# Kernel tuning notes

Measured on AMD Instinct MI355X. Metric: run time of the kernel, lower is better.

Reference implementation:

```python
import jax, jax.numpy as jnp
import numpy as np

T, N, E, IN, H, H2, H3, B, AF = 12, 50000, 800000, 12, 128, 64, 32, 4096, 10
BN_EPS = 1e-5


def _gin_mlp(h, w1, b1, g, be, rm, rv, w2, b2):
    # Linear -> ReLU -> BatchNorm1d (eval: running stats) -> Dropout(eval=id) -> Linear -> ReLU
    h = jax.nn.relu(h @ w1.T + b1)
    h = (h - rm) * (g * jax.lax.rsqrt(rv + BN_EPS)) + be
    return jax.nn.relu(h @ w2.T + b2)


def _gin_conv(x, edge_src, edge_dst, mlp_params):
    # GINConv with eps=0: MLP(x + sum_{j in N(i)} x_j), scatter-add over edges
    agg = jax.ops.segment_sum(x[edge_src], edge_dst, num_segments=x.shape[0])
    return _gin_mlp(x + agg, *mlp_params)


def _gru(xs, wih, whh, bih, bhh):
    # torch.nn.GRU, 1 layer, h0 = zeros. xs: [T, N, H_in]
    h0 = jnp.zeros((xs.shape[1], whh.shape[1]), xs.dtype)

    def step(h, x):
        gi = x @ wih.T + bih
        gh = h @ whh.T + bhh
        ir, iz, inn = jnp.split(gi, 3, axis=-1)
        hr, hz, hn = jnp.split(gh, 3, axis=-1)
        r = jax.nn.sigmoid(ir + hr)
        z = jax.nn.sigmoid(iz + hz)
        n = jnp.tanh(inn + r * hn)
        h_new = (1.0 - z) * n + z * h
        return h_new, h_new

    h_last, ys = jax.lax.scan(step, h0, xs)
    return ys, h_last


def _forward(floats, edge_src, edge_dst, target_idx):
    (x_seq, apart_feature,
     c1_w1, c1_b1, c1_g, c1_be, c1_rm, c1_rv, c1_w2, c1_b2,
     c2_w1, c2_b1, c2_g, c2_be, c2_rm, c2_rv, c2_w2, c2_b2,
     gru_wih, gru_whh, gru_bih, gru_bhh,
     fc1_w, fc1_b, fc2_w, fc2_b, fc3_w, fc3_b) = floats

    c1 = (c1_w1, c1_b1, c1_g, c1_be, c1_rm, c1_rv, c1_w2, c1_b2)
    c2 = (c2_w1, c2_b1, c2_g, c2_be, c2_rm, c2_rv, c2_w2, c2_b2)

    # conv1 per time slot (lax.map keeps the E x H gather intermediate per-step)
    # extra torch.relu after conv1 is a no-op since the MLP ends in ReLU
    emb = jax.lax.map(lambda xt: _gin_conv(xt, edge_src, edge_dst, c1), x_seq)
    seq, _ = _gru(emb, gru_wih, gru_whh, gru_bih, gru_bhh)
    emb2 = jax.lax.map(lambda xt: _gin_conv(xt, edge_src, edge_dst, c2), seq)
    _, h_last = _gru(emb2, gru_wih, gru_whh, gru_bih, gru_bhh)  # same GRU weights reused

    feat = jnp.concatenate([h_last[target_idx], apart_feature], axis=1)
    h = jax.nn.leaky_relu(feat @ fc1_w.T + fc1_b, negative_slope=0.1)
    h = jax.nn.leaky_relu(h @ fc2_w.T + fc2_b, negative_slope=0.05)
    return h @ fc3_w.T + fc3_b  # [B, 1]


def setup_inputs() -> dict:
    key = jax.random.key(0)
    ks = jax.random.split(key, 24)
    f32 = jnp.float32
    w = lambda i, shape, fan: jax.random.normal(ks[i], shape, f32) * (1.0 / np.sqrt(fan))
    return {
        "x_seq": jax.random.normal(ks[0], (T, N, IN), f32),
        "apart_feature": jax.random.normal(ks[1], (B, AF), f32),
        "edge_src": jax.random.randint(ks[2], (E,), 0, N, jnp.int32),
        "edge_dst": jax.random.randint(ks[3], (E,), 0, N, jnp.int32),
        "target_idx": jax.random.randint(ks[4], (B,), 0, N, jnp.int32),
        # conv1 MLP
        "c1_w1": w(5, (H, IN), IN), "c1_b1": jnp.zeros((H,), f32),
        "c1_g": jnp.ones((H,), f32), "c1_be": jnp.zeros((H,), f32),
        "c1_rm": jnp.zeros((H,), f32), "c1_rv": jnp.ones((H,), f32),
        "c1_w2": w(6, (H, H), H), "c1_b2": jnp.zeros((H,), f32),
        # conv2 MLP
        "c2_w1": w(7, (H, H), H), "c2_b1": jnp.zeros((H,), f32),
        "c2_g": jnp.ones((H,), f32), "c2_be": jnp.zeros((H,), f32),
        "c2_rm": jnp.zeros((H,), f32), "c2_rv": jnp.ones((H,), f32),
        "c2_w2": w(8, (H, H), H), "c2_b2": jnp.zeros((H,), f32),
        # shared GRU
        "gru_wih": w(9, (3 * H, H), H), "gru_whh": w(10, (3 * H, H), H),
        "gru_bih": jnp.zeros((3 * H,), f32), "gru_bhh": jnp.zeros((3 * H,), f32),
        # head
        "fc1_w": w(11, (H2, H + AF), H + AF), "fc1_b": jnp.zeros((H2,), f32),
        "fc2_w": w(12, (H3, H2), H2), "fc2_b": jnp.zeros((H3,), f32),
        "fc3_w": w(13, (1, H3), H3), "fc3_b": jnp.zeros((1,), f32),
    }


def reference(x_seq, apart_feature,
              c1_w1, c1_b1, c1_g, c1_be, c1_rm, c1_rv, c1_w2, c1_b2,
              c2_w1, c2_b1, c2_g, c2_be, c2_rm, c2_rv, c2_w2, c2_b2,
              gru_wih, gru_whh, gru_bih, gru_bhh,
              fc1_w, fc1_b, fc2_w, fc2_b, fc3_w, fc3_b,
              edge_src, edge_dst, target_idx):
    floats = (x_seq, apart_feature,
              c1_w1, c1_b1, c1_g, c1_be, c1_rm, c1_rv, c1_w2, c1_b2,
              c2_w1, c2_b1, c2_g, c2_be, c2_rm, c2_rv, c2_w2, c2_b2,
              gru_wih, gru_whh, gru_bih, gru_bhh,
              fc1_w, fc1_b, fc2_w, fc2_b, fc3_w, fc3_b)
    return _forward(floats, edge_src, edge_dst, target_idx)
```

## Files before the change

kernel.cpp:

```cpp
#include <hip/hip_runtime.h>

#define T_STEPS 12
#define NN      50000
#define EE      800000
#define IN_F    12
#define HID     128
#define G3      384
#define BB      4096
#define AF_     10
#define BN_EPS  1e-5f
#define LPAD    136
#define NBLK    ((NN + 63) / 64)

typedef unsigned short ushort_t;
typedef __attribute__((ext_vector_type(8))) short bf16x8;
typedef __attribute__((ext_vector_type(4))) float f32x4;

#define MFMA(a, b, c) __builtin_amdgcn_mfma_f32_16x16x32_bf16((a), (b), (c), 0, 0, 0)
#define L2E 1.4426950408889634f

__device__ inline float b2f(ushort_t u) { return __uint_as_float(((unsigned)u) << 16); }
__device__ inline float b2f_lo(unsigned u) { return __uint_as_float(u << 16); }
__device__ inline float b2f_hi(unsigned u) { return __uint_as_float(u & 0xffff0000u); }
__device__ inline ushort_t f2b(float f) {
    unsigned u = __float_as_uint(f);
    return (ushort_t)((u + 0x7fffu + ((u >> 16) & 1u)) >> 16);
}
__device__ inline float sigm(float x) {
    return __builtin_amdgcn_rcpf(1.f + __builtin_amdgcn_exp2f(-x * L2E));
}
__device__ inline float ftanh(float x) {
    float xx = fminf(fmaxf(x, -15.f), 15.f);
    float t = __builtin_amdgcn_exp2f(2.f * L2E * xx);
    return (t - 1.f) * __builtin_amdgcn_rcpf(t + 1.f);
}
__device__ inline void v4add(float4& a, const float4 b) {
    a.x += b.x; a.y += b.y; a.z += b.z; a.w += b.w;
}

#define ALIGN_UP(x) (((x) + 255) & ~(size_t)255)
#define SZ_DEG    ALIGN_UP((size_t)NN * 4)
#define SZ_RP     ALIGN_UP((size_t)(NN + 1) * 4)
#define SZ_CUR    ALIGN_UP((size_t)NN * 4)
#define SZ_COL    ALIGN_UP((size_t)EE * 4)
#define SZ_X12A   ALIGN_UP((size_t)T_STEPS * NN * IN_F * 4)
#define SZ_EMB    ALIGN_UP((size_t)T_STEPS * NN * HID * 2)
#define SZ_NHB    ALIGN_UP((size_t)NN * HID * 2)
#define SZ_W128   ALIGN_UP((size_t)HID * HID * 2)
#define SZ_WGRU   ALIGN_UP((size_t)G3 * HID * 2)
#define WS_NEED   (SZ_DEG + SZ_RP + SZ_CUR + SZ_COL + SZ_X12A + SZ_EMB + 3 * SZ_NHB + 3 * SZ_W128 + 2 * SZ_WGRU)

__device__ __align__(256) char g_static_pool[WS_NEED];

__global__ void zero_out_kernel(float* out, int n) {
    int i = blockIdx.x * blockDim.x + threadIdx.x;
    if (i < n) out[i] = 0.f;
}

__global__ void cvt5_kernel(const float* s0, ushort_t* d0, int n0,
                            const float* s1, ushort_t* d1, int n1,
                            const float* s2, ushort_t* d2, int n2,
                            const float* s3, ushort_t* d3, int n3,
                            const float* s4, ushort_t* d4, int n4) {
    int i = blockIdx.x * blockDim.x + threadIdx.x;
    if (i < n0) d0[i] = f2b(s0[i]);
    i -= n0;
    if (i >= 0 && i < n1) d1[i] = f2b(s1[i]);
    i -= n1;
    if (i >= 0 && i < n2) d2[i] = f2b(s2[i]);
    i -= n2;
    if (i >= 0 && i < n3) d3[i] = f2b(s3[i]);
    i -= n3;
    if (i >= 0 && i < n4) d4[i] = f2b(s4[i]);
}

__global__ void init_kernel(int* deg, ushort_t* h1, ushort_t* h2) {
    int i = blockIdx.x * blockDim.x + threadIdx.x;
    if (i < NN) deg[i] = 0;
    if (i < NN * HID) { h1[i] = 0; h2[i] = 0; }
}

__global__ void hist_kernel(const int* __restrict__ dst, int* __restrict__ deg, int E) {
    int e = blockIdx.x * blockDim.x + threadIdx.x;
    if (e < E) {
        unsigned d = (unsigned)dst[e];
        if (d < NN) atomicAdd(&deg[d], 1);
    }
}

__global__ __launch_bounds__(1024) void scan_kernel(const int* __restrict__ deg,
                                                    int* __restrict__ row_ptr,
                                                    int* __restrict__ cursor, int n) {
    __shared__ int wsum[16];
    __shared__ int carry_s;
    int tid = threadIdx.x;
    int wid = tid >> 6, lane = tid & 63;
    if (tid == 0) { carry_s = 0; row_ptr[0] = 0; }
    __syncthreads();
    for (int base = 0; base < n; base += 1024) {
        int i = base + tid;
        int v = (i < n) ? deg[i] : 0;
        int x = v;
#pragma unroll
        for (int off = 1; off < 64; off <<= 1) {
            int t = __shfl_up(x, (unsigned)off);
            if (lane >= off) x += t;
        }
        if (lane == 63) wsum[wid] = x;
        __syncthreads();
        if (tid == 0) {
            int a = 0;
#pragma unroll
            for (int w = 0; w < 16; ++w) { int t = wsum[w]; wsum[w] = a; a += t; }
        }
        __syncthreads();
        int incl = carry_s + wsum[wid] + x;
        if (i < n) {
            row_ptr[i + 1] = incl;
            cursor[i] = incl - v;
        }
        __syncthreads();
        if (tid == 1023) carry_s = incl;
        __syncthreads();
    }
}

__global__ void scatter_kernel(const int* __restrict__ src, const int* __restrict__ dst,
                               int* __restrict__ cursor, int* __restrict__ col, int E) {
    int e = blockIdx.x * blockDim.x + threadIdx.x;
    if (e < E) {
        unsigned d = (unsigned)dst[e];
        if (d < NN) {
            int pos = atomicAdd(&cursor[d], 1);
            if ((unsigned)pos < (unsigned)EE) col[pos] = src[e];
        }
    }
}

__global__ void agg12v_kernel(const float* __restrict__ x_seq, const int* __restrict__ rp,
                              const int* __restrict__ col, float* __restrict__ xin12_all, int E) {
    int g = blockIdx.x * blockDim.x + threadIdx.x;
    if (g >= T_STEPS * NN) return;
    int t = g / NN;
    int i = g - t * NN;
    const float* xt = x_seq + (size_t)t * NN * IN_F;
    const float4* pr = (const float4*)(xt + (size_t)i * IN_F);
    float4 a0 = pr[0], a1 = pr[1], a2 = pr[2];
    int e0 = rp[i], e1 = rp[i + 1];
    if (e1 > E) e1 = E;
    int e = e0;
    for (; e + 1 < e1; e += 2) {
        unsigned c0 = (unsigned)col[e], c1 = (unsigned)col[e + 1];
        c0 = (c0 < NN) ? c0 : 0; c1 = (c1 < NN) ? c1 : 0;
        const float4* p0 = (const float4*)(xt + (size_t)c0 * IN_F);
        const float4* p1 = (const float4*)(xt + (size_t)c1 * IN_F);
        float4 b0 = p0[0], b1 = p0[1], b2 = p0[2];
        float4 d0 = p1[0], d1 = p1[1], d2 = p1[2];
        v4add(a0, b0); v4add(a1, b1); v4add(a2, b2);
        v4add(a0, d0); v4add(a1, d1); v4add(a2, d2);
    }
    for (; e < e1; ++e) {
        unsigned c = (unsigned)col[e];
        if (c < NN) {
            const float4* pn = (const float4*)(xt + (size_t)c * IN_F);
            v4add(a0, pn[0]); v4add(a1, pn[1]); v4add(a2, pn[2]);
        }
    }
    float4* po = (float4*)(xin12_all + (size_t)g * IN_F);
    po[0] = a0; po[1] = a1; po[2] = a2;
}

__global__ __launch_bounds__(512) void conv1c_all_kernel(const float* __restrict__ xin12_all,
                                                         ushort_t* __restrict__ emb,
                                                         const float* __restrict__ W1, const float* __restrict__ b1,
                                                         const float* __restrict__ gg, const float* __restrict__ be,
                                                         const float* __restrict__ rm, const float* __restrict__ rv,
                                                         const ushort_t* __restrict__ w2b, const float* __restrict__ b2) {
    __shared__ float xs[64][IN_F + 1];
    __shared__ ushort_t l1[64][LPAD];
    int t = blockIdx.y;
    const float* xt = xin12_all + (size_t)t * NN * IN_F;
    ushort_t* et = emb + (size_t)t * NN * HID;
    int tid = threadIdx.x;
    int r0 = blockIdx.x * 64;
    for (int u = tid; u < 64 * IN_F; u += 512) {
        int r = u / IN_F, f = u - r * IN_F;
        int row = r0 + r;
        xs[r][f] = (row < NN) ? xt[(size_t)row * IN_F + f] : 0.f;
    }
    __syncthreads();
    {
        int j = tid & 127, rb = tid >> 7;
        float sc = gg[j] * rsqrtf(rv[j] + BN_EPS);
        float sh = be[j] - rm[j] * sc;
        float bj = b1[j];
        float wreg[IN_F];
#pragma unroll
        for (int k = 0; k < IN_F; ++k) wreg[k] = W1[j * IN_F + k];
#pragma unroll
        for (int q = 0; q < 16; ++q) {
            int r = rb + q * 4;
            float s = bj;
#pragma unroll
            for (int k = 0; k < IN_F; ++k) s += xs[r][k] * wreg[k];
            s = fmaxf(s, 0.f);
            l1[r][j] = f2b(s * sc + sh);
        }
    }
    __syncthreads();
    {
        int wave = tid >> 6, lane = tid & 63, li = lane & 15, ks = lane >> 4;
        int jc = wave * 16 + li;
        const ushort_t* pw = w2b + (size_t)jc * HID + ks * 8;
        f32x4 A0 = {0,0,0,0}, A1 = {0,0,0,0}, A2 = {0,0,0,0}, A3 = {0,0,0,0};
#pragma unroll
        for (int k0 = 0; k0 < HID; k0 += 32) {
            bf16x8 wf = *(const bf16x8*)(pw + k0);
            bf16x8 a0 = *(const bf16x8*)&l1[li][ks * 8 + k0];
            bf16x8 a1 = *(const bf16x8*)&l1[li + 16][ks * 8 + k0];
            bf16x8 a2 = *(const bf16x8*)&l1[li + 32][ks * 8 + k0];
            bf16x8 a3 = *(const bf16x8*)&l1[li + 48][ks * 8 + k0];
            A0 = MFMA(a0, wf, A0); A1 = MFMA(a1, wf, A1);
            A2 = MFMA(a2, wf, A2); A3 = MFMA(a3, wf, A3);
        }
        float bj = b2[jc];
#pragma unroll
        for (int q = 0; q < 4; ++q) {
            int rA = r0 + ks * 4 + q, rB = rA + 16, rC = rA + 32, rD = rA + 48;
            if (rA < NN) et[(size_t)rA * HID + jc] = f2b(fmaxf(A0[q] + bj, 0.f));
            if (rB < NN) et[(size_t)rB * HID + jc] = f2b(fmaxf(A1[q] + bj, 0.f));
            if (rC < NN) et[(size_t)rC * HID + jc] = f2b(fmaxf(A2[q] + bj, 0.f));
            if (rD < NN) et[(size_t)rD * HID + jc] = f2b(fmaxf(A3[q] + bj, 0.f));
        }
    }
}

__device__ __forceinline__ void gru_body(const ushort_t* __restrict__ x,
                                         ushort_t* __restrict__ h,
                                         const ushort_t* __restrict__ wih,
                                         const ushort_t* __restrict__ whh,
                                         const float* __restrict__ bih,
                                         const float* __restrict__ bhh, int blk) {
    int tid = threadIdx.x;
    int wave = tid >> 6, lane = tid & 63, li = lane & 15, ks = lane >> 4;
    int r0 = blk * 64;
    int jc = wave * 16 + li;
    const ushort_t* px[4];
    const ushort_t* ph[4];
#pragma unroll
    for (int tt = 0; tt < 4; ++tt) {
        int ra = min(r0 + tt * 16 + li, NN - 1);
        px[tt] = x + (size_t)ra * HID + ks * 8;
        ph[tt] = h + (size_t)ra * HID + ks * 8;
    }
    const ushort_t* pwr = wih + (size_t)jc * HID + ks * 8;
    const ushort_t* pwz = wih + (size_t)(HID + jc) * HID + ks * 8;
    const ushort_t* pwn = wih + (size_t)(2 * HID + jc) * HID + ks * 8;
    const ushort_t* pvr = whh + (size_t)jc * HID + ks * 8;
    const ushort_t* pvz = whh + (size_t)(HID + jc) * HID + ks * 8;
    const ushort_t* pvn = whh + (size_t)(2 * HID + jc) * HID + ks * 8;
    f32x4 Ir[4], Iz[4], In[4], Hr[4], Hz[4], Hn[4];
#pragma unroll
    for (int tt = 0; tt < 4; ++tt) {
        Ir[tt] = (f32x4){0,0,0,0}; Iz[tt] = (f32x4){0,0,0,0}; In[tt] = (f32x4){0,0,0,0};
        Hr[tt] = (f32x4){0,0,0,0}; Hz[tt] = (f32x4){0,0,0,0}; Hn[tt] = (f32x4){0,0,0,0};
    }
#pragma unroll
    for (int k0 = 0; k0 < HID; k0 += 32) {
        bf16x8 wr = *(const bf16x8*)(pwr + k0);
        bf16x8 wz = *(const bf16x8*)(pwz + k0);
        bf16x8 wn = *(const bf16x8*)(pwn + k0);
        bf16x8 vr = *(const bf16x8*)(pvr + k0);
        bf16x8 vz = *(const bf16x8*)(pvz + k0);
        bf16x8 vn = *(const bf16x8*)(pvn + k0);
#pragma unroll
        for (int tt = 0; tt < 4; ++tt) {
            bf16x8 xf = *(const bf16x8*)(px[tt] + k0);
            bf16x8 hf = *(const bf16x8*)(ph[tt] + k0);
            Ir[tt] = MFMA(xf, wr, Ir[tt]);
            Iz[tt] = MFMA(xf, wz, Iz[tt]);
            In[tt] = MFMA(xf, wn, In[tt]);
            Hr[tt] = MFMA(hf, vr, Hr[tt]);
            Hz[tt] = MFMA(hf, vz, Hz[tt]);
            Hn[tt] = MFMA(hf, vn, Hn[tt]);
        }
    }
    float bi_r = bih[jc], bi_z = bih[HID + jc], bi_n = bih[2 * HID + jc];
    float bh_r = bhh[jc], bh_z = bhh[HID + jc], bh_n = bhh[2 * HID + jc];
    float hold[4][4];
#pragma unroll
    for (int tt = 0; tt < 4; ++tt)
#pragma unroll
        for (int q = 0; q < 4; ++q) {
            int rr = min(r0 + tt * 16 + ks * 4 + q, NN - 1);
            hold[tt][q] = b2f(h[(size_t)rr * HID + jc]);
        }
    __syncthreads();
#pragma unroll
    for (int tt = 0; tt < 4; ++tt)
#pragma unroll
        for (int q = 0; q < 4; ++q) {
            int row = r0 + tt * 16 + ks * 4 + q;
            float rg = sigm(Ir[tt][q] + bi_r + Hr[tt][q] + bh_r);
            float zg = sigm(Iz[tt][q] + bi_z + Hz[tt][q] + bh_z);
            float ng = ftanh(In[tt][q] + bi_n + rg * (Hn[tt][q] + bh_n));
            float hv = (1.f - zg) * ng + zg * hold[tt][q];
            if (row < NN) h[(size_t)row * HID + jc] = f2b(hv);
        }
}

__device__ __forceinline__ void mega2_body(const ushort_t* __restrict__ xin2,
                                           ushort_t* __restrict__ h2,
                                           const ushort_t* __restrict__ w1b, const float* __restrict__ b1,
                                           const float* __restrict__ gg, const float* __restrict__ be,
                                           const float* __restrict__ rm, const float* __restrict__ rv,
                                           const ushort_t* __restrict__ w2b, const float* __restrict__ b2,
                                           const ushort_t* __restrict__ wih, const ushort_t* __restrict__ whh,
                                           const float* __restrict__ bih, const float* __restrict__ bhh, int blk) {
    __shared__ ushort_t bufA[64][LPAD];
    __shared__ ushort_t bufB[64][LPAD];
    int tid = threadIdx.x;
    int wave = tid >> 6, lane = tid & 63, li = lane & 15, ks = lane >> 4;
    int r0 = blk * 64;
    int jc = wave * 16 + li;
    f32x4 Hr[4], Hz[4], Hn[4], C1[4];
#pragma unroll
    for (int tt = 0; tt < 4; ++tt) {
        Hr[tt] = (f32x4){0,0,0,0}; Hz[tt] = (f32x4){0,0,0,0};
        Hn[tt] = (f32x4){0,0,0,0}; C1[tt] = (f32x4){0,0,0,0};
    }
    {
        const ushort_t* pw1 = w1b + (size_t)jc * HID + ks * 8;
        const ushort_t* pvr = whh + (size_t)jc * HID + ks * 8;
        const ushort_t* pvz = whh + (size_t)(HID + jc) * HID + ks * 8;
        const ushort_t* pvn = whh + (size_t)(2 * HID + jc) * HID + ks * 8;
        const ushort_t* pa[4];
        const ushort_t* ph[4];
#pragma unroll
        for (int tt = 0; tt < 4; ++tt) {
            int ra = min(r0 + tt * 16 + li, NN - 1);
            pa[tt] = xin2 + (size_t)ra * HID + ks * 8;
            ph[tt] = h2 + (size_t)ra * HID + ks * 8;
        }
#pragma unroll
        for (int k0 = 0; k0 < HID; k0 += 32) {
            bf16x8 w1f = *(const bf16x8*)(pw1 + k0);
            bf16x8 vr = *(const bf16x8*)(pvr + k0);
            bf16x8 vz = *(const bf16x8*)(pvz + k0);
            bf16x8 vn = *(const bf16x8*)(pvn + k0);
#pragma unroll
            for (int tt = 0; tt < 4; ++tt) {
                bf16x8 af = *(const bf16x8*)(pa[tt] + k0);
                bf16x8 hf = *(const bf16x8*)(ph[tt] + k0);
                C1[tt] = MFMA(af, w1f, C1[tt]);
                Hr[tt] = MFMA(hf, vr, Hr[tt]);
                Hz[tt] = MFMA(hf, vz, Hz[tt]);
                Hn[tt] = MFMA(hf, vn, Hn[tt]);
            }
        }
    }
    float hold[4][4];
#pragma unroll
    for (int tt = 0; tt < 4; ++tt)
#pragma unroll
        for (int q = 0; q < 4; ++q) {
            int rr = min(r0 + tt * 16 + ks * 4 + q, NN - 1);
            hold[tt][q] = b2f(h2[(size_t)rr * HID + jc]);
        }
    {
        float sc = gg[jc] * rsqrtf(rv[jc] + BN_EPS);
        float sh = be[jc] - rm[jc] * sc;
        float bj = b1[jc];
#pragma unroll
        for (int tt = 0; tt < 4; ++tt)
#pragma unroll
            for (int q = 0; q < 4; ++q)
                bufB[tt * 16 + ks * 4 + q][jc] = f2b(fmaxf(C1[tt][q] + bj, 0.f) * sc + sh);
    }
    __syncthreads();
    {
        const ushort_t* pw2 = w2b + (size_t)jc * HID + ks * 8;
        f32x4 C2[4];
#pragma unroll
        for (int tt = 0; tt < 4; ++tt) C2[tt] = (f32x4){0,0,0,0};
#pragma unroll
        for (int k0 = 0; k0 < HID; k0 += 32) {
            bf16x8 wf = *(const bf16x8*)(pw2 + k0);
#pragma unroll
            for (int tt = 0; tt < 4; ++tt) {
                bf16x8 af = *(const bf16x8*)&bufB[li + 16 * tt][ks * 8 + k0];
                C2[tt] = MFMA(af, wf, C2[tt]);
            }
        }
        float bj = b2[jc];
#pragma unroll
        for (int tt = 0; tt < 4; ++tt)
#pragma unroll
            for (int q = 0; q < 4; ++q)
                bufA[tt * 16 + ks * 4 + q][jc] = f2b(fmaxf(C2[tt][q] + bj, 0.f));
    }
    __syncthreads();
    {
        const ushort_t* pwr = wih + (size_t)jc * HID + ks * 8;
        const ushort_t* pwz = wih + (size_t)(HID + jc) * HID + ks * 8;
        const ushort_t* pwn = wih + (size_t)(2 * HID + jc) * HID + ks * 8;
        f32x4 Ir[4], Iz[4], In[4];
#pragma unroll
        for (int tt = 0; tt < 4; ++tt) {
            Ir[tt] = (f32x4){0,0,0,0}; Iz[tt] = (f32x4){0,0,0,0}; In[tt] = (f32x4){0,0,0,0};
        }
#pragma unroll
        for (int k0 = 0; k0 < HID; k0 += 32) {
            bf16x8 wr = *(const bf16x8*)(pwr + k0);
            bf16x8 wz = *(const bf16x8*)(pwz + k0);
            bf16x8 wn = *(const bf16x8*)(pwn + k0);
#pragma unroll
            for (int tt = 0; tt < 4; ++tt) {
                bf16x8 xf = *(const bf16x8*)&bufA[li + 16 * tt][ks * 8 + k0];
                Ir[tt] = MFMA(xf, wr, Ir[tt]);
                Iz[tt] = MFMA(xf, wz, Iz[tt]);
                In[tt] = MFMA(xf, wn, In[tt]);
            }
        }
        float bi_r = bih[jc], bi_z = bih[HID + jc], bi_n = bih[2 * HID + jc];
        float bh_r = bhh[jc], bh_z = bhh[HID + jc], bh_n = bhh[2 * HID + jc];
#pragma unroll
        for (int tt = 0; tt < 4; ++tt)
#pragma unroll
            for (int q = 0; q < 4; ++q) {
                int row = r0 + tt * 16 + ks * 4 + q;
                float rg = sigm(Ir[tt][q] + bi_r + Hr[tt][q] + bh_r);
                float zg = sigm(Iz[tt][q] + bi_z + Hz[tt][q] + bh_z);
                float ng = ftanh(In[tt][q] + bi_n + rg * (Hn[tt][q] + bh_n));
                float hv = (1.f - zg) * ng + zg * hold[tt][q];
                if (row < NN) h2[(size_t)row * HID + jc] = f2b(hv);
            }
    }
}

__global__ __launch_bounds__(512) void gru_step_kernel(const ushort_t* __restrict__ x, ushort_t* __restrict__ h,
                                                       const ushort_t* __restrict__ wih, const ushort_t* __restrict__ whh,
                                                       const float* __restrict__ bih, const float* __restrict__ bhh) {
    gru_body(x, h, wih, whh, bih, bhh, blockIdx.x);
}

__global__ __launch_bounds__(512) void mega2_kernel(const ushort_t* __restrict__ xin2, ushort_t* __restrict__ h2,
                                                    const ushort_t* __restrict__ w1b, const float* __restrict__ b1,
                                                    const float* __restrict__ gg, const float* __restrict__ be,
                                                    const float* __restrict__ rm, const float* __restrict__ rv,
                                                    const ushort_t* __restrict__ w2b, const float* __restrict__ b2,
                                                    const ushort_t* __restrict__ wih, const ushort_t* __restrict__ whh,
                                                    const float* __restrict__ bih, const float* __restrict__ bhh) {
    mega2_body(xin2, h2, w1b, b1, gg, be, rm, rv, w2b, b2, wih, whh, bih, bhh, blockIdx.x);
}

__global__ __launch_bounds__(512) void fused_mg_kernel(const ushort_t* __restrict__ xin2, ushort_t* __restrict__ h2,
                                                       const ushort_t* __restrict__ w1b, const float* __restrict__ b1,
                                                       const float* __restrict__ gg, const float* __restrict__ be,
                                                       const float* __restrict__ rm, const float* __restrict__ rv,
                                                       const ushort_t* __restrict__ w2b, const float* __restrict__ b2,
                                                       const ushort_t* __restrict__ wih, const ushort_t* __restrict__ whh,
                                                       const float* __restrict__ bih, const float* __restrict__ bhh,
                                                       const ushort_t* __restrict__ emb_next, ushort_t* __restrict__ h1) {
    int b = blockIdx.x;
    if (b < NBLK) {
        mega2_body(xin2, h2, w1b, b1, gg, be, rm, rv, w2b, b2, wih, whh, bih, bhh, b);
    } else {
        gru_body(emb_next, h1, wih, whh, bih, bhh, b - NBLK);
    }
}

__global__ __launch_bounds__(256) void agg128b_kernel(const ushort_t* __restrict__ x,
                                                      const int* __restrict__ rp,
                                                      const int* __restrict__ col,
                                                      ushort_t* __restrict__ out, int E) {
    int node = (blockIdx.x * 256 + threadIdx.x) >> 6;
    int lane = threadIdx.x & 63;
    if (node >= NN) return;
    unsigned v = *(const unsigned*)(x + (size_t)node * HID + lane * 2);
    float s0 = b2f_lo(v);
    float s1 = b2f_hi(v);
    int e0 = rp[node], e1 = rp[node + 1];
    if (e1 > E) e1 = E;
    int e = e0;
    for (; e + 3 < e1; e += 4) {
        unsigned c0 = (unsigned)col[e], c1 = (unsigned)col[e + 1];
        unsigned c2 = (unsigned)col[e + 2], c3 = (unsigned)col[e + 3];
        c0 = (c0 < NN) ? c0 : 0; c1 = (c1 < NN) ? c1 : 0;
        c2 = (c2 < NN) ? c2 : 0; c3 = (c3 < NN) ? c3 : 0;
        unsigned u0 = *(const unsigned*)(x + (size_t)c0 * HID + lane * 2);
        unsigned u1 = *(const unsigned*)(x + (size_t)c1 * HID + lane * 2);
        unsigned u2 = *(const unsigned*)(x + (size_t)c2 * HID + lane * 2);
        unsigned u3 = *(const unsigned*)(x + (size_t)c3 * HID + lane * 2);
        s0 += b2f_lo(u0) + b2f_lo(u1) + b2f_lo(u2) + b2f_lo(u3);
        s1 += b2f_hi(u0) + b2f_hi(u1) + b2f_hi(u2) + b2f_hi(u3);
    }
    for (; e < e1; ++e) {
        unsigned c = (unsigned)col[e];
        if (c < NN) {
            unsigned u = *(const unsigned*)(x + (size_t)c * HID + lane * 2);
            s0 += b2f_lo(u);
            s1 += b2f_hi(u);
        }
    }
    unsigned o = (unsigned)f2b(s0) | ((unsigned)f2b(s1) << 16);
    *(unsigned*)(out + (size_t)node * HID + lane * 2) = o;
}

__global__ __launch_bounds__(64) void head_kernel(const ushort_t* __restrict__ h2, const int* __restrict__ tidx,
                                                  const float* __restrict__ apart,
                                                  const float* __restrict__ w1, const float* __restrict__ b1,
                                                  const float* __restrict__ w2, const float* __restrict__ b2,
                                                  const float* __restrict__ w3, const float* __restrict__ b3,
                                                  float* __restrict__ out) {
    __shared__ float feat[HID + AF_];
    __shared__ float o1[64];
    __shared__ float o2[32];
    int b = blockIdx.x;
    int t = threadIdx.x;
    unsigned node = (unsigned)tidx[b];
    if (node >= NN) node = 0;
    for (int k = t; k < HID; k += 64) feat[k] = b2f(h2[(size_t)node * HID + k]);
    if (t < AF_) feat[HID + t] = apart[(size_t)b * AF_ + t];
    __syncthreads();
    {
        float s = b1[t];
        for (int k = 0; k < HID + AF_; ++k) s += feat[k] * w1[t * (HID + AF_) + k];
        o1[t] = (s > 0.f) ? s : 0.1f * s;
    }
    __syncthreads();
    if (t < 32) {
        float s = b2[t];
        for (int k = 0; k < 64; ++k) s += o1[k] * w2[t * 64 + k];
        o2[t] = (s > 0.f) ? s : 0.05f * s;
    }
    __syncthreads();
    if (t == 0) {
        float s = b3[0];
        for (int k = 0; k < 32; ++k) s += o2[k] * w3[k];
        out[b] = s;
    }
}

extern "C" void kernel_launch(void* const* d_in, const int* in_sizes, int n_in,
                              void* d_out, int out_size, void* d_ws, size_t ws_size,
                              hipStream_t stream) {
    int ie_src = -1, ie_dst = -1, ie_tidx = -1, iw0 = -1;
    bool ok = false;
    if (n_in >= 31 && in_sizes[0] == T_STEPS * NN * IN_F && in_sizes[1] == BB * AF_) {
        if (in_sizes[2] > 100000 && in_sizes[3] == in_sizes[2] && in_sizes[4] == BB &&
            in_sizes[5] == HID * IN_F && in_sizes[11] == HID * HID &&
            in_sizes[21] == G3 * HID && in_sizes[22] == G3 * HID &&
            in_sizes[25] == 64 * (HID + AF_)) {
            ie_src = 2; ie_dst = 3; ie_tidx = 4; iw0 = 5; ok = true;
        } else if (in_sizes[2] == HID * IN_F && in_sizes[8] == HID * HID &&
                   in_sizes[18] == G3 * HID && in_sizes[19] == G3 * HID &&
                   in_sizes[22] == 64 * (HID + AF_) &&
                   in_sizes[28] > 100000 && in_sizes[29] == in_sizes[28] && in_sizes[30] == BB) {
            iw0 = 2; ie_src = 28; ie_dst = 29; ie_tidx = 30; ok = true;
        }
    }
    if (!ok) {
        zero_out_kernel<<<(out_size + 255) / 256, 256, 0, stream>>>((float*)d_out, out_size);
        return;
    }

    const float* x_seq  = (const float*)d_in[0];
    const float* apart  = (const float*)d_in[1];
    const int*   e_src  = (const int*)d_in[ie_src];
    const int*   e_dst  = (const int*)d_in[ie_dst];
    const int*   t_idx  = (const int*)d_in[ie_tidx];
    const float* c1_w1 = (const float*)d_in[iw0 + 0];
    const float* c1_b1 = (const float*)d_in[iw0 + 1];
    const float* c1_g  = (const float*)d_in[iw0 + 2];
    const float* c1_be = (const float*)d_in[iw0 + 3];
    const float* c1_rm = (const float*)d_in[iw0 + 4];
    const float* c1_rv = (const float*)d_in[iw0 + 5];
    const float* c1_w2 = (const float*)d_in[iw0 + 6];
    const float* c1_b2 = (const float*)d_in[iw0 + 7];
    const float* c2_w1 = (const float*)d_in[iw0 + 8];
    const float* c2_b1 = (const float*)d_in[iw0 + 9];
    const float* c2_g  = (const float*)d_in[iw0 + 10];
    const float* c2_be = (const float*)d_in[iw0 + 11];
    const float* c2_rm = (const float*)d_in[iw0 + 12];
    const float* c2_rv = (const float*)d_in[iw0 + 13];
    const float* c2_w2 = (const float*)d_in[iw0 + 14];
    const float* c2_b2 = (const float*)d_in[iw0 + 15];
    const float* g_wih = (const float*)d_in[iw0 + 16];
    const float* g_whh = (const float*)d_in[iw0 + 17];
    const float* g_bih = (const float*)d_in[iw0 + 18];
    const float* g_bhh = (const float*)d_in[iw0 + 19];
    const float* f1_w  = (const float*)d_in[iw0 + 20];
    const float* f1_b  = (const float*)d_in[iw0 + 21];
    const float* f2_w  = (const float*)d_in[iw0 + 22];
    const float* f2_b  = (const float*)d_in[iw0 + 23];
    const float* f3_w  = (const float*)d_in[iw0 + 24];
    const float* f3_b  = (const float*)d_in[iw0 + 25];

    int E = in_sizes[ie_src];
    if (E > EE) E = EE;

    char* base;
    if (ws_size >= WS_NEED) {
        base = (char*)d_ws;
    } else {
        void* sp = nullptr;
        hipGetSymbolAddress(&sp, HIP_SYMBOL(g_static_pool));
        if (sp == nullptr) {
            zero_out_kernel<<<(out_size + 255) / 256, 256, 0, stream>>>((float*)d_out, out_size);
            return;
        }
        base = (char*)sp;
    }
    size_t off = 0;
    auto nxt = [&](size_t bytes) { char* p = base + off; off += bytes; return p; };
    int*      deg      = (int*)nxt(SZ_DEG);
    int*      row_ptr  = (int*)nxt(SZ_RP);
    int*      cursor   = (int*)nxt(SZ_CUR);
    int*      col      = (int*)nxt(SZ_COL);
    float*    xin12a   = (float*)nxt(SZ_X12A);
    ushort_t* emb      = (ushort_t*)nxt(SZ_EMB);
    ushort_t* xin2     = (ushort_t*)nxt(SZ_NHB);
    ushort_t* h1       = (ushort_t*)nxt(SZ_NHB);
    ushort_t* h2       = (ushort_t*)nxt(SZ_NHB);
    ushort_t* wb_c1w2  = (ushort_t*)nxt(SZ_W128);
    ushort_t* wb_c2w1  = (ushort_t*)nxt(SZ_W128);
    ushort_t* wb_c2w2  = (ushort_t*)nxt(SZ_W128);
    ushort_t* wb_wih   = (ushort_t*)nxt(SZ_WGRU);
    ushort_t* wb_whh   = (ushort_t*)nxt(SZ_WGRU);

    const int NW = 3 * HID * HID + 2 * G3 * HID;
    cvt5_kernel<<<(NW + 255) / 256, 256, 0, stream>>>(c1_w2, wb_c1w2, HID * HID,
                                                      c2_w1, wb_c2w1, HID * HID,
                                                      c2_w2, wb_c2w2, HID * HID,
                                                      g_wih, wb_wih, G3 * HID,
                                                      g_whh, wb_whh, G3 * HID);

    init_kernel<<<(NN * HID + 255) / 256, 256, 0, stream>>>(deg, h1, h2);

    hist_kernel<<<(E + 255) / 256, 256, 0, stream>>>(e_dst, deg, E);
    scan_kernel<<<1, 1024, 0, stream>>>(deg, row_ptr, cursor, NN);
    scatter_kernel<<<(E + 255) / 256, 256, 0, stream>>>(e_src, e_dst, cursor, col, E);

    agg12v_kernel<<<(T_STEPS * NN + 255) / 256, 256, 0, stream>>>(x_seq, row_ptr, col, xin12a, E);
    conv1c_all_kernel<<<dim3(NBLK, T_STEPS), 512, 0, stream>>>(xin12a, emb,
                                                               c1_w1, c1_b1, c1_g, c1_be, c1_rm, c1_rv,
                                                               wb_c1w2, c1_b2);

    gru_step_kernel<<<NBLK, 512, 0, stream>>>(emb, h1, wb_wih, wb_whh, g_bih, g_bhh);
    agg128b_kernel<<<(NN * 64 + 255) / 256, 256, 0, stream>>>(h1, row_ptr, col, xin2, E);
    for (int t = 0; t < T_STEPS - 1; ++t) {
        fused_mg_kernel<<<2 * NBLK, 512, 0, stream>>>(xin2, h2,
                                                      wb_c2w1, c2_b1, c2_g, c2_be, c2_rm, c2_rv,
                                                      wb_c2w2, c2_b2,
                                                      wb_wih, wb_whh, g_bih, g_bhh,
                                                      emb + (size_t)(t + 1) * NN * HID, h1);
        agg128b_kernel<<<(NN * 64 + 255) / 256, 256, 0, stream>>>(h1, row_ptr, col, xin2, E);
    }
    mega2_kernel<<<NBLK, 512, 0, stream>>>(xin2, h2,
                                           wb_c2w1, c2_b1, c2_g, c2_be, c2_rm, c2_rv,
                                           wb_c2w2, c2_b2,
                                           wb_wih, wb_whh, g_bih, g_bhh);

    head_kernel<<<BB, 64, 0, stream>>>(h2, t_idx, apart, f1_w, f1_b, f2_w, f2_b, f3_w, f3_b, (float*)d_out);
}
```

Before: 2.351 ms.

## Interleave per-step conv1 and input aggregation into layer-2 recurrence kernels

The upfront all-timestep input aggregation and conv1 launches are split per time plane. Each plane's work is folded into the fusedA kernel alongside the 128-wide neighbour aggregation of the recurrent loop, so that lightweight conv1 work fills the GPU during the latency-bound aggregation steps. Shared memory moves to explicit pools so different bodies can share one kernel. The cost is more complex block dispatch and a larger shared footprint in the aggregation kernel, which may lower its occupancy.

```diff
diff --git a/kernel.cpp b/kernel.cpp
--- a/kernel.cpp
+++ b/kernel.cpp
@@ -11,6 +11,8 @@
 #define BN_EPS  1e-5f
 #define LPAD    136
 #define NBLK    ((NN + 63) / 64)
+#define AGGB    ((NN + 7) / 8)
+#define AGVB    ((NN + 511) / 512)
 
 typedef unsigned short ushort_t;
 typedef __attribute__((ext_vector_type(8))) short bf16x8;
@@ -49,6 +51,9 @@
 #define SZ_W128   ALIGN_UP((size_t)HID * HID * 2)
 #define SZ_WGRU   ALIGN_UP((size_t)G3 * HID * 2)
 #define WS_NEED   (SZ_DEG + SZ_RP + SZ_CUR + SZ_COL + SZ_X12A + SZ_EMB + 3 * SZ_NHB + 3 * SZ_W128 + 2 * SZ_WGRU)
+
+#define POOL_C1   (64 * (IN_F + 1) * 4 + 64 * LPAD * 2)
+#define POOL_M2   (2 * 64 * LPAD * 2)
 
 __device__ __align__(256) char g_static_pool[WS_NEED];
 
@@ -137,13 +142,13 @@
     }
 }
 
-__global__ void agg12v_kernel(const float* __restrict__ x_seq, const int* __restrict__ rp,
-                              const int* __restrict__ col, float* __restrict__ xin12_all, int E) {
-    int g = blockIdx.x * blockDim.x + threadIdx.x;
-    if (g >= T_STEPS * NN) return;
-    int t = g / NN;
-    int i = g - t * NN;
-    const float* xt = x_seq + (size_t)t * NN * IN_F;
+__device__ __forceinline__ void agg12v_body(const float* __restrict__ x_seq, const int* __restrict__ rp,
+                                            const int* __restrict__ col, float* __restrict__ xin12_all,
+                                            int E, int plane, int blk) {
+    int tid = threadIdx.x;
+    int i = blk * 512 + tid;
+    if (i >= NN) return;
+    const float* xt = x_seq + (size_t)plane * NN * IN_F;
     const float4* pr = (const float4*)(xt + (size_t)i * IN_F);
     float4 a0 = pr[0], a1 = pr[1], a2 = pr[2];
     int e0 = rp[i], e1 = rp[i + 1];
@@ -166,23 +171,29 @@
             v4add(a0, pn[0]); v4add(a1, pn[1]); v4add(a2, pn[2]);
         }
     }
-    float4* po = (float4*)(xin12_all + (size_t)g * IN_F);
+    float4* po = (float4*)(xin12_all + ((size_t)plane * NN + i) * IN_F);
     po[0] = a0; po[1] = a1; po[2] = a2;
 }
 
-__global__ __launch_bounds__(512) void conv1c_all_kernel(const float* __restrict__ xin12_all,
-                                                         ushort_t* __restrict__ emb,
-                                                         const float* __restrict__ W1, const float* __restrict__ b1,
-                                                         const float* __restrict__ gg, const float* __restrict__ be,
-                                                         const float* __restrict__ rm, const float* __restrict__ rv,
-                                                         const ushort_t* __restrict__ w2b, const float* __restrict__ b2) {
-    __shared__ float xs[64][IN_F + 1];
-    __shared__ ushort_t l1[64][LPAD];
-    int t = blockIdx.y;
-    const float* xt = xin12_all + (size_t)t * NN * IN_F;
-    ushort_t* et = emb + (size_t)t * NN * HID;
+__global__ __launch_bounds__(512) void agg12v_kernel(const float* __restrict__ x_seq, const int* __restrict__ rp,
+                                                     const int* __restrict__ col, float* __restrict__ xin12_all,
+                                                     int E, int plane0) {
+    agg12v_body(x_seq, rp, col, xin12_all, E, plane0 + blockIdx.y, blockIdx.x);
+}
+
+__device__ __forceinline__ void conv1c_body(const float* __restrict__ xin12_all,
+                                            ushort_t* __restrict__ emb,
+                                            const float* __restrict__ W1, const float* __restrict__ b1,
+                                            const float* __restrict__ gg, const float* __restrict__ be,
+                                            const float* __restrict__ rm, const float* __restrict__ rv,
+                                            const ushort_t* __restrict__ w2b, const float* __restrict__ b2,
+                                            int plane, int blk, char* pool) {
+    float (*xs)[IN_F + 1] = (float(*)[IN_F + 1])pool;
+    ushort_t (*l1)[LPAD] = (ushort_t(*)[LPAD])(pool + 64 * (IN_F + 1) * 4);
+    const float* xt = xin12_all + (size_t)plane * NN * IN_F;
+    ushort_t* et = emb + (size_t)plane * NN * HID;
     int tid = threadIdx.x;
-    int r0 = blockIdx.x * 64;
+    int r0 = blk * 64;
     for (int u = tid; u < 64 * IN_F; u += 512) {
         int r = u / IN_F, f = u - r * IN_F;
         int row = r0 + r;
@@ -233,6 +244,17 @@
             if (rD < NN) et[(size_t)rD * HID + jc] = f2b(fmaxf(A3[q] + bj, 0.f));
         }
     }
+}
+
+__global__ __launch_bounds__(512) void conv1c_kernel(const float* __restrict__ xin12_all,
+                                                     ushort_t* __restrict__ emb,
+                                                     const float* __restrict__ W1, const float* __restrict__ b1,
+                                                     const float* __restrict__ gg, const float* __restrict__ be,
+                                                     const float* __restrict__ rm, const float* __restrict__ rv,
+                                                     const ushort_t* __restrict__ w2b, const float* __restrict__ b2,
+                                                     int plane) {
+    __shared__ __align__(16) char pool[POOL_C1];
+    conv1c_body(xin12_all, emb, W1, b1, gg, be, rm, rv, w2b, b2, plane, blockIdx.x, pool);
 }
 
 __device__ __forceinline__ void gru_body(const ushort_t* __restrict__ x,
@@ -316,9 +338,10 @@
                                            const float* __restrict__ rm, const float* __restrict__ rv,
                                            const ushort_t* __restrict__ w2b, const float* __restrict__ b2,
                                            const ushort_t* __restrict__ wih, const ushort_t* __restrict__ whh,
-                                           const float* __restrict__ bih, const float* __restrict__ bhh, int blk) {
-    __shared__ ushort_t bufA[64][LPAD];
-    __shared__ ushort_t bufB[64][LPAD];
+                                           const float* __restrict__ bih, const float* __restrict__ bhh,
+                                           int blk, char* pool) {
+    ushort_t (*bufA)[LPAD] = (ushort_t(*)[LPAD])pool;
+    ushort_t (*bufB)[LPAD] = (ushort_t(*)[LPAD])(pool + 64 * LPAD * 2);
     int tid = threadIdx.x;
     int wave = tid >> 6, lane = tid & 63, li = lane & 15, ks = lane >> 4;
     int r0 = blk * 64;
@@ -438,43 +461,11 @@
     }
 }
 
-__global__ __launch_bounds__(512) void gru_step_kernel(const ushort_t* __restrict__ x, ushort_t* __restrict__ h,
-                                                       const ushort_t* __restrict__ wih, const ushort_t* __restrict__ whh,
-                                                       const float* __restrict__ bih, const float* __restrict__ bhh) {
-    gru_body(x, h, wih, whh, bih, bhh, blockIdx.x);
-}
-
-__global__ __launch_bounds__(512) void mega2_kernel(const ushort_t* __restrict__ xin2, ushort_t* __restrict__ h2,
-                                                    const ushort_t* __restrict__ w1b, const float* __restrict__ b1,
-                                                    const float* __restrict__ gg, const float* __restrict__ be,
-                                                    const float* __restrict__ rm, const float* __restrict__ rv,
-                                                    const ushort_t* __restrict__ w2b, const float* __restrict__ b2,
-                                                    const ushort_t* __restrict__ wih, const ushort_t* __restrict__ whh,
-                                                    const float* __restrict__ bih, const float* __restrict__ bhh) {
-    mega2_body(xin2, h2, w1b, b1, gg, be, rm, rv, w2b, b2, wih, whh, bih, bhh, blockIdx.x);
-}
-
-__global__ __launch_bounds__(512) void fused_mg_kernel(const ushort_t* __restrict__ xin2, ushort_t* __restrict__ h2,
-                                                       const ushort_t* __restrict__ w1b, const float* __restrict__ b1,
-                                                       const float* __restrict__ gg, const float* __restrict__ be,
-                                                       const float* __restrict__ rm, const float* __restrict__ rv,
-                                                       const ushort_t* __restrict__ w2b, const float* __restrict__ b2,
-                                                       const ushort_t* __restrict__ wih, const ushort_t* __restrict__ whh,
-                                                       const float* __restrict__ bih, const float* __restrict__ bhh,
-                                                       const ushort_t* __restrict__ emb_next, ushort_t* __restrict__ h1) {
-    int b = blockIdx.x;
-    if (b < NBLK) {
-        mega2_body(xin2, h2, w1b, b1, gg, be, rm, rv, w2b, b2, wih, whh, bih, bhh, b);
-    } else {
-        gru_body(emb_next, h1, wih, whh, bih, bhh, b - NBLK);
-    }
-}
-
-__global__ __launch_bounds__(256) void agg128b_kernel(const ushort_t* __restrict__ x,
-                                                      const int* __restrict__ rp,
-                                                      const int* __restrict__ col,
-                                                      ushort_t* __restrict__ out, int E) {
-    int node = (blockIdx.x * 256 + threadIdx.x) >> 6;
+__device__ __forceinline__ void agg128b_body(const ushort_t* __restrict__ x,
+                                             const int* __restrict__ rp,
+                                             const int* __restrict__ col,
+                                             ushort_t* __restrict__ out, int E, int blk) {
+    int node = blk * 8 + (threadIdx.x >> 6);
     int lane = threadIdx.x & 63;
     if (node >= NN) return;
     unsigned v = *(const unsigned*)(x + (size_t)node * HID + lane * 2);
@@ -505,6 +496,68 @@
     }
     unsigned o = (unsigned)f2b(s0) | ((unsigned)f2b(s1) << 16);
     *(unsigned*)(out + (size_t)node * HID + lane * 2) = o;
+}
+
+__global__ __launch_bounds__(512) void fusedA_kernel(const ushort_t* __restrict__ h1,
+                                                     const int* __restrict__ rp, const int* __restrict__ col,
+                                                     ushort_t* __restrict__ xin2, int E,
+                                                     const float* __restrict__ xin12_all, ushort_t* __restrict__ emb,
+                                                     const float* __restrict__ W1, const float* __restrict__ b1,
+                                                     const float* __restrict__ gg, const float* __restrict__ be,
+                                                     const float* __restrict__ rm, const float* __restrict__ rv,
+                                                     const ushort_t* __restrict__ w2b, const float* __restrict__ b2,
+                                                     const float* __restrict__ x_seq, float* __restrict__ xin12_out,
+                                                     int c1_plane, int ag_plane) {
+    __shared__ __align__(16) char pool[POOL_C1];
+    int b = blockIdx.x;
+    if (b < AGGB) {
+        agg128b_body(h1, rp, col, xin2, E, b);
+        return;
+    }
+    b -= AGGB;
+    if (c1_plane >= 0) {
+        if (b < NBLK) {
+            conv1c_body(xin12_all, emb, W1, b1, gg, be, rm, rv, w2b, b2, c1_plane, b, pool);
+            return;
+        }
+        b -= NBLK;
+    }
+    if (ag_plane >= 0 && b < AGVB)
+        agg12v_body(x_seq, rp, col, xin12_out, E, ag_plane, b);
+}
+
+__global__ __launch_bounds__(512) void fusedL_kernel(const ushort_t* __restrict__ xin2, ushort_t* __restrict__ h2,
+                                                     const ushort_t* __restrict__ w1b, const float* __restrict__ b1,
+                                                     const float* __restrict__ gg, const float* __restrict__ be,
+                                                     const float* __restrict__ rm, const float* __restrict__ rv,
+                                                     const ushort_t* __restrict__ w2b, const float* __restrict__ b2,
+                                                     const ushort_t* __restrict__ wih, const ushort_t* __restrict__ whh,
+                                                     const float* __restrict__ bih, const float* __restrict__ bhh,
+                                                     const ushort_t* __restrict__ emb_next, ushort_t* __restrict__ h1) {
+    __shared__ __align__(16) char pool[POOL_M2];
+    int b = blockIdx.x;
+    if (b < NBLK) {
+        mega2_body(xin2, h2, w1b, b1, gg, be, rm, rv, w2b, b2, wih, whh, bih, bhh, b, pool);
+    } else {
+        gru_body(emb_next, h1, wih, whh, bih, bhh, b - NBLK);
+    }
+}
+
+__global__ __launch_bounds__(512) void gru_step_kernel(const ushort_t* __restrict__ x, ushort_t* __restrict__ h,
+                                                       const ushort_t* __restrict__ wih, const ushort_t* __restrict__ whh,
+                                                       const float* __restrict__ bih, const float* __restrict__ bhh) {
+    gru_body(x, h, wih, whh, bih, bhh, blockIdx.x);
+}
+
+__global__ __launch_bounds__(512) void mega2_kernel(const ushort_t* __restrict__ xin2, ushort_t* __restrict__ h2,
+                                                    const ushort_t* __restrict__ w1b, const float* __restrict__ b1,
+                                                    const float* __restrict__ gg, const float* __restrict__ be,
+                                                    const float* __restrict__ rm, const float* __restrict__ rv,
+                                                    const ushort_t* __restrict__ w2b, const float* __restrict__ b2,
+                                                    const ushort_t* __restrict__ wih, const ushort_t* __restrict__ whh,
+                                                    const float* __restrict__ bih, const float* __restrict__ bhh) {
+    __shared__ __align__(16) char pool[POOL_M2];
+    mega2_body(xin2, h2, w1b, b1, gg, be, rm, rv, w2b, b2, wih, whh, bih, bhh, blockIdx.x, pool);
 }
 
 __global__ __launch_bounds__(64) void head_kernel(const ushort_t* __restrict__ h2, const int* __restrict__ tidx,
@@ -642,21 +695,31 @@
     scan_kernel<<<1, 1024, 0, stream>>>(deg, row_ptr, cursor, NN);
     scatter_kernel<<<(E + 255) / 256, 256, 0, stream>>>(e_src, e_dst, cursor, col, E);
 
-    agg12v_kernel<<<(T_STEPS * NN + 255) / 256, 256, 0, stream>>>(x_seq, row_ptr, col, xin12a, E);
-    conv1c_all_kernel<<<dim3(NBLK, T_STEPS), 512, 0, stream>>>(xin12a, emb,
-                                                               c1_w1, c1_b1, c1_g, c1_be, c1_rm, c1_rv,
-                                                               wb_c1w2, c1_b2);
-
+    agg12v_kernel<<<dim3(AGVB, 2), 512, 0, stream>>>(x_seq, row_ptr, col, xin12a, E, 0);
+    conv1c_kernel<<<NBLK, 512, 0, stream>>>(xin12a, emb, c1_w1, c1_b1, c1_g, c1_be, c1_rm, c1_rv,
+                                            wb_c1w2, c1_b2, 0);
     gru_step_kernel<<<NBLK, 512, 0, stream>>>(emb, h1, wb_wih, wb_whh, g_bih, g_bhh);
-    agg128b_kernel<<<(NN * 64 + 255) / 256, 256, 0, stream>>>(h1, row_ptr, col, xin2, E);
+
     for (int t = 0; t < T_STEPS - 1; ++t) {
-        fused_mg_kernel<<<2 * NBLK, 512, 0, stream>>>(xin2, h2,
-                                                      wb_c2w1, c2_b1, c2_g, c2_be, c2_rm, c2_rv,
-                                                      wb_c2w2, c2_b2,
-                                                      wb_wih, wb_whh, g_bih, g_bhh,
-                                                      emb + (size_t)(t + 1) * NN * HID, h1);
-        agg128b_kernel<<<(NN * 64 + 255) / 256, 256, 0, stream>>>(h1, row_ptr, col, xin2, E);
-    }
+        int c1p = (t + 1 <= T_STEPS - 1) ? (t + 1) : -1;
+        int agp = (t + 2 <= T_STEPS - 1) ? (t + 2) : -1;
+        int grid = AGGB + (c1p >= 0 ? NBLK : 0) + (agp >= 0 ? AGVB : 0);
+        fusedA_kernel<<<grid, 512, 0, stream>>>(h1, row_ptr, col, xin2, E,
+                                                xin12a, emb,
+                                                c1_w1, c1_b1, c1_g, c1_be, c1_rm, c1_rv,
+                                                wb_c1w2, c1_b2,
+                                                x_seq, xin12a, c1p, agp);
+        fusedL_kernel<<<2 * NBLK, 512, 0, stream>>>(xin2, h2,
+                                                    wb_c2w1, c2_b1, c2_g, c2_be, c2_rm, c2_rv,
+                                                    wb_c2w2, c2_b2,
+                                                    wb_wih, wb_whh, g_bih, g_bhh,
+                                                    emb + (size_t)(t + 1) * NN * HID, h1);
+    }
+    fusedA_kernel<<<AGGB, 512, 0, stream>>>(h1, row_ptr, col, xin2, E,
+                                            xin12a, emb,
+                                            c1_w1, c1_b1, c1_g, c1_be, c1_rm, c1_rv,
+                                            wb_c1w2, c1_b2,
+                                            x_seq, xin12a, -1, -1);
     mega2_kernel<<<NBLK, 512, 0, stream>>>(xin2, h2,
                                            wb_c2w1, c2_b1, c2_g, c2_be, c2_rm, c2_rv,
                                            wb_c2w2, c2_b2,
```

New measurement: 2.547 ms. 8.3% more time.

## Transpose input sequence to node-major layout for one-wavefront-per-node aggregation

Applied to the files above, without the earlier changes.

Adds a transpose kernel that rearranges x_seq from [T,N,F] to node-major [N,T*F]. Aggregation then runs once across all time steps, with one wavefront per node reading a contiguous 576-byte row per neighbor, instead of one thread per (t,node) re-reading the CSR for every step. The aim is coalesced neighbor gathers and a single pass over the edge list, at the cost of an extra transpose pass and a strided read in conv1.

```diff
diff --git a/kernel.cpp b/kernel.cpp
--- a/kernel.cpp
+++ b/kernel.cpp
@@ -4,6 +4,7 @@
 #define NN      50000
 #define EE      800000
 #define IN_F    12
+#define TF12    (T_STEPS * IN_F)
 #define HID     128
 #define G3      384
 #define BB      4096
@@ -34,21 +35,18 @@
     float t = __builtin_amdgcn_exp2f(2.f * L2E * xx);
     return (t - 1.f) * __builtin_amdgcn_rcpf(t + 1.f);
 }
-__device__ inline void v4add(float4& a, const float4 b) {
-    a.x += b.x; a.y += b.y; a.z += b.z; a.w += b.w;
-}
 
 #define ALIGN_UP(x) (((x) + 255) & ~(size_t)255)
 #define SZ_DEG    ALIGN_UP((size_t)NN * 4)
 #define SZ_RP     ALIGN_UP((size_t)(NN + 1) * 4)
 #define SZ_CUR    ALIGN_UP((size_t)NN * 4)
 #define SZ_COL    ALIGN_UP((size_t)EE * 4)
-#define SZ_X12A   ALIGN_UP((size_t)T_STEPS * NN * IN_F * 4)
+#define SZ_XT     ALIGN_UP((size_t)NN * TF12 * 4)
 #define SZ_EMB    ALIGN_UP((size_t)T_STEPS * NN * HID * 2)
 #define SZ_NHB    ALIGN_UP((size_t)NN * HID * 2)
 #define SZ_W128   ALIGN_UP((size_t)HID * HID * 2)
 #define SZ_WGRU   ALIGN_UP((size_t)G3 * HID * 2)
-#define WS_NEED   (SZ_DEG + SZ_RP + SZ_CUR + SZ_COL + SZ_X12A + SZ_EMB + 3 * SZ_NHB + 3 * SZ_W128 + 2 * SZ_WGRU)
+#define WS_NEED   (SZ_DEG + SZ_RP + SZ_CUR + SZ_COL + 2 * SZ_XT + SZ_EMB + 3 * SZ_NHB + 3 * SZ_W128 + 2 * SZ_WGRU)
 
 __device__ __align__(256) char g_static_pool[WS_NEED];
 
@@ -137,40 +135,56 @@
     }
 }
 
-__global__ void agg12v_kernel(const float* __restrict__ x_seq, const int* __restrict__ rp,
-                              const int* __restrict__ col, float* __restrict__ xin12_all, int E) {
+__global__ void transpose_x_kernel(const float* __restrict__ x_seq, float* __restrict__ xT) {
     int g = blockIdx.x * blockDim.x + threadIdx.x;
-    if (g >= T_STEPS * NN) return;
-    int t = g / NN;
-    int i = g - t * NN;
-    const float* xt = x_seq + (size_t)t * NN * IN_F;
-    const float4* pr = (const float4*)(xt + (size_t)i * IN_F);
-    float4 a0 = pr[0], a1 = pr[1], a2 = pr[2];
-    int e0 = rp[i], e1 = rp[i + 1];
+    if (g >= NN * TF12) return;
+    int n = g / TF12;
+    int u = g - n * TF12;
+    int t = u / IN_F;
+    int f = u - t * IN_F;
+    xT[g] = x_seq[(size_t)t * NN * IN_F + (size_t)n * IN_F + f];
+}
+
+__global__ __launch_bounds__(512) void agg12t_kernel(const float* __restrict__ xT,
+                                                     const int* __restrict__ rp,
+                                                     const int* __restrict__ col,
+                                                     float* __restrict__ xagg, int E) {
+    int node = blockIdx.x * 8 + (threadIdx.x >> 6);
+    int lane = threadIdx.x & 63;
+    if (node >= NN) return;
+    const float2* pself = (const float2*)(xT + (size_t)node * TF12);
+    float2 a = pself[lane];
+    float a2 = (lane < 16) ? xT[(size_t)node * TF12 + 128 + lane] : 0.f;
+    int e0 = rp[node], e1 = rp[node + 1];
     if (e1 > E) e1 = E;
     int e = e0;
     for (; e + 1 < e1; e += 2) {
         unsigned c0 = (unsigned)col[e], c1 = (unsigned)col[e + 1];
         c0 = (c0 < NN) ? c0 : 0; c1 = (c1 < NN) ? c1 : 0;
-        const float4* p0 = (const float4*)(xt + (size_t)c0 * IN_F);
-        const float4* p1 = (const float4*)(xt + (size_t)c1 * IN_F);
-        float4 b0 = p0[0], b1 = p0[1], b2 = p0[2];
-        float4 d0 = p1[0], d1 = p1[1], d2 = p1[2];
-        v4add(a0, b0); v4add(a1, b1); v4add(a2, b2);
-        v4add(a0, d0); v4add(a1, d1); v4add(a2, d2);
+        const float2* p0 = (const float2*)(xT + (size_t)c0 * TF12);
+        const float2* p1 = (const float2*)(xT + (size_t)c1 * TF12);
+        float2 v0 = p0[lane];
+        float2 v1 = p1[lane];
+        a.x += v0.x + v1.x;
+        a.y += v0.y + v1.y;
+        if (lane < 16)
+            a2 += xT[(size_t)c0 * TF12 + 128 + lane] + xT[(size_t)c1 * TF12 + 128 + lane];
     }
     for (; e < e1; ++e) {
         unsigned c = (unsigned)col[e];
         if (c < NN) {
-            const float4* pn = (const float4*)(xt + (size_t)c * IN_F);
-            v4add(a0, pn[0]); v4add(a1, pn[1]); v4add(a2, pn[2]);
-        }
-    }
-    float4* po = (float4*)(xin12_all + (size_t)g * IN_F);
-    po[0] = a0; po[1] = a1; po[2] = a2;
-}
-
-__global__ __launch_bounds__(512) void conv1c_all_kernel(const float* __restrict__ xin12_all,
+            const float2* pn = (const float2*)(xT + (size_t)c * TF12);
+            float2 v = pn[lane];
+            a.x += v.x;
+            a.y += v.y;
+            if (lane < 16) a2 += xT[(size_t)c * TF12 + 128 + lane];
+        }
+    }
+    ((float2*)(xagg + (size_t)node * TF12))[lane] = a;
+    if (lane < 16) xagg[(size_t)node * TF12 + 128 + lane] = a2;
+}
+
+__global__ __launch_bounds__(512) void conv1c_all_kernel(const float* __restrict__ xagg,
                                                          ushort_t* __restrict__ emb,
                                                          const float* __restrict__ W1, const float* __restrict__ b1,
                                                          const float* __restrict__ gg, const float* __restrict__ be,
@@ -179,14 +193,13 @@
     __shared__ float xs[64][IN_F + 1];
     __shared__ ushort_t l1[64][LPAD];
     int t = blockIdx.y;
-    const float* xt = xin12_all + (size_t)t * NN * IN_F;
     ushort_t* et = emb + (size_t)t * NN * HID;
     int tid = threadIdx.x;
     int r0 = blockIdx.x * 64;
     for (int u = tid; u < 64 * IN_F; u += 512) {
         int r = u / IN_F, f = u - r * IN_F;
         int row = r0 + r;
-        xs[r][f] = (row < NN) ? xt[(size_t)row * IN_F + f] : 0.f;
+        xs[r][f] = (row < NN) ? xagg[(size_t)row * TF12 + t * IN_F + f] : 0.f;
     }
     __syncthreads();
     {
@@ -618,7 +631,8 @@
     int*      row_ptr  = (int*)nxt(SZ_RP);
     int*      cursor   = (int*)nxt(SZ_CUR);
     int*      col      = (int*)nxt(SZ_COL);
-    float*    xin12a   = (float*)nxt(SZ_X12A);
+    float*    xT       = (float*)nxt(SZ_XT);
+    float*    xagg     = (float*)nxt(SZ_XT);
     ushort_t* emb      = (ushort_t*)nxt(SZ_EMB);
     ushort_t* xin2     = (ushort_t*)nxt(SZ_NHB);
     ushort_t* h1       = (ushort_t*)nxt(SZ_NHB);
@@ -642,8 +656,9 @@
     scan_kernel<<<1, 1024, 0, stream>>>(deg, row_ptr, cursor, NN);
     scatter_kernel<<<(E + 255) / 256, 256, 0, stream>>>(e_src, e_dst, cursor, col, E);
 
-    agg12v_kernel<<<(T_STEPS * NN + 255) / 256, 256, 0, stream>>>(x_seq, row_ptr, col, xin12a, E);
-    conv1c_all_kernel<<<dim3(NBLK, T_STEPS), 512, 0, stream>>>(xin12a, emb,
+    transpose_x_kernel<<<(NN * TF12 + 255) / 256, 256, 0, stream>>>(x_seq, xT);
+    agg12t_kernel<<<(NN + 7) / 8, 512, 0, stream>>>(xT, row_ptr, col, xagg, E);
+    conv1c_all_kernel<<<dim3(NBLK, T_STEPS), 512, 0, stream>>>(xagg, emb,
                                                                c1_w1, c1_b1, c1_g, c1_be, c1_rm, c1_rv,
                                                                wb_c1w2, c1_b2);
 
```

New measurement: 2.270 ms. -3.5%, faster.
